# Optimization experiments

Hardware: AMD Instinct MI355X
Metric: run time of the kernel (lower is better)

## Reference

```python
import jax, jax.numpy as jnp
import numpy as np

B, C, H, W = 8, 256, 128, 128


def _conv1x1(x, w, b):
    # x: [B,C,H,W], w: [Cout,Cin], b: [Cout]
    return jnp.einsum('oc,bchw->bohw', w, x) + b[None, :, None, None]


def setup_inputs() -> dict:
    key = jax.random.key(0)
    ks = jax.random.split(key, 12)
    s = 1.0 / np.sqrt(C)
    d = {
        'x0': jax.random.normal(ks[0], (B, C, H, W), jnp.float32),
        'x1': jax.random.normal(ks[1], (B, C, H, W), jnp.float32),
        'g_w': jax.random.uniform(ks[2], (C, C), jnp.float32, -s, s),
        'g_b': jax.random.uniform(ks[3], (C,), jnp.float32, -s, s),
        'theta_w': jax.random.uniform(ks[4], (C, C), jnp.float32, -s, s),
        'theta_b': jax.random.uniform(ks[5], (C,), jnp.float32, -s, s),
        'phi_w': jax.random.uniform(ks[6], (C, C), jnp.float32, -s, s),
        'phi_b': jax.random.uniform(ks[7], (C,), jnp.float32, -s, s),
        # Original inits W to zero; use small random weights so output/grads are nontrivial.
        'W_w': jax.random.uniform(ks[8], (C, C), jnp.float32, -s, s) * 0.1,
        'W_b': jax.random.uniform(ks[9], (C,), jnp.float32, -s, s) * 0.1,
    }
    return d


def reference(x0, x1, g_w, g_b, theta_w, theta_b, phi_w, phi_b, W_w, W_b):
    b, c, h, w = x0.shape
    n = h * w
    g_x = _conv1x1(x0, g_w, g_b).reshape(b, c, n)        # [B,C,N]
    theta_x = _conv1x1(x1, theta_w, theta_b).reshape(b, c, n)  # [B,C,N]
    phi_x = _conv1x1(x0, phi_w, phi_b).reshape(b, c, n)   # [B,C,N]
    # f = theta_x @ phi_x^T : [B,C,C]; NO scaling, softmax over dim=1 (columns-normalized)
    f = jnp.einsum('bcn,bdn->bcd', theta_x, phi_x)
    f_div_C = jax.nn.softmax(f, axis=1)
    y = jnp.einsum('bcd,bdn->bcn', f_div_C, g_x)          # [B,C,N]
    # Faithful to torch: permute to [B,N,C] contiguous, then view as [B,C,H,W]
    y = jnp.transpose(y, (0, 2, 1)).reshape(b, c, h, w)
    return _conv1x1(y, W_w, W_b)
```

## Files before the change

### kernel.cpp

```cpp
#include <hip/hip_runtime.h>
#include <hip/hip_bf16.h>
#include <stdint.h>


typedef __attribute__((ext_vector_type(4))) float f32x4;
typedef __attribute__((ext_vector_type(8))) short s16x8;

#define MFMA16(A,B,C) __builtin_amdgcn_mfma_f32_16x16x32_bf16((A),(B),(C),0,0,0)

__device__ __forceinline__ short f2bf(float f) {
    union { float f; uint32_t u; } v; v.f = f;
    uint32_t r = v.u + 0x7fffu + ((v.u >> 16) & 1u);
    return (short)(r >> 16);
}
__device__ __forceinline__ float bf2f(short h) {
    union { uint32_t u; float f; } v; v.u = ((uint32_t)(uint16_t)h) << 16;
    return v.f;
}
__device__ __forceinline__ s16x8 pack2(f32x4 a, f32x4 b) {
    s16x8 r;
    r[0]=f2bf(a.x); r[1]=f2bf(a.y); r[2]=f2bf(a.z); r[3]=f2bf(a.w);
    r[4]=f2bf(b.x); r[5]=f2bf(b.y); r[6]=f2bf(b.z); r[7]=f2bf(b.w);
    return r;
}
__device__ __forceinline__ void pack2_hl(f32x4 a, f32x4 b, s16x8& hi, s16x8& lo) {
    float v[8] = {a.x,a.y,a.z,a.w,b.x,b.y,b.z,b.w};
#pragma unroll
    for (int i=0;i<8;++i) {
        short h = f2bf(v[i]);
        hi[i] = h;
        lo[i] = f2bf(v[i] - bf2f(h));
    }
}
__device__ __forceinline__ float hsum4(f32x4 v){ return (v.x+v.y)+(v.z+v.w); }

__global__ __launch_bounds__(256) void k0_prep(
    const float* __restrict__ g_w, const float* __restrict__ W_w,
    short* __restrict__ gwT, short* __restrict__ Wwb,
    float* __restrict__ s0, float* __restrict__ s1)
{
    int gid = blockIdx.x * 256 + threadIdx.x;
    int d = gid >> 8, e = gid & 255;
    gwT[e*256 + d] = f2bf(g_w[gid]);
    Wwb[gid] = f2bf(W_w[gid]);
    if (gid < 2048) { s0[gid] = 0.f; s1[gid] = 0.f; }
}

__global__ __launch_bounds__(256) void k1_gram(
    const float* __restrict__ x0, const float* __restrict__ x1,
    float* __restrict__ partial, float* __restrict__ s0, float* __restrict__ s1)
{
    __shared__ short Ah[128*40], Al[128*40], Bh[128*40], Bl[128*40];
    int bid = blockIdx.x;
    int ij = bid & 3, ch = (bid >> 2) & 15, b = bid >> 6;
    int i0 = (ij >> 1) * 128, j0 = (ij & 1) * 128, k0 = ch * 1024;
    int tid = threadIdx.x;
    int w = tid >> 6, lane = tid & 63;
    int wr = (w >> 1) * 64, wc = (w & 1) * 64;
    int quad = lane >> 4, l16 = lane & 15;
    int srow = tid >> 1, skk = (tid & 1) * 16;

    const float* pa = x1 + (size_t)(b*256 + i0 + srow)*16384 + k0 + skk;
    const float* pb = x0 + (size_t)(b*256 + j0 + srow)*16384 + k0 + skk;

    f32x4 acc[4][4];
#pragma unroll
    for (int i=0;i<4;i++)
#pragma unroll
    for (int j=0;j<4;j++) acc[i][j] = f32x4{0.f,0.f,0.f,0.f};

    float sumA = 0.f, sumB = 0.f;

    for (int s = 0; s < 32; ++s) {
        f32x4 av[4], bv[4];
#pragma unroll
        for (int q=0;q<4;++q) { av[q] = *(const f32x4*)(pa + q*4); bv[q] = *(const f32x4*)(pb + q*4); }
        pa += 32; pb += 32;
#pragma unroll
        for (int q=0;q<4;++q) { sumA += hsum4(av[q]); sumB += hsum4(bv[q]); }
        __syncthreads();
        s16x8 h, l;
        pack2_hl(av[0], av[1], h, l);
        ((s16x8*)(Ah + srow*40 + skk))[0] = h; ((s16x8*)(Al + srow*40 + skk))[0] = l;
        pack2_hl(av[2], av[3], h, l);
        ((s16x8*)(Ah + srow*40 + skk))[1] = h; ((s16x8*)(Al + srow*40 + skk))[1] = l;
        pack2_hl(bv[0], bv[1], h, l);
        ((s16x8*)(Bh + srow*40 + skk))[0] = h; ((s16x8*)(Bl + srow*40 + skk))[0] = l;
        pack2_hl(bv[2], bv[3], h, l);
        ((s16x8*)(Bh + srow*40 + skk))[1] = h; ((s16x8*)(Bl + srow*40 + skk))[1] = l;
        __syncthreads();
        s16x8 ah[4], al[4], bh[4], bl[4];
#pragma unroll
        for (int mt=0; mt<4; ++mt) {
            ah[mt] = *(const s16x8*)(Ah + (wr + mt*16 + l16)*40 + quad*8);
            al[mt] = *(const s16x8*)(Al + (wr + mt*16 + l16)*40 + quad*8);
        }
#pragma unroll
        for (int nt=0; nt<4; ++nt) {
            bh[nt] = *(const s16x8*)(Bh + (wc + nt*16 + l16)*40 + quad*8);
            bl[nt] = *(const s16x8*)(Bl + (wc + nt*16 + l16)*40 + quad*8);
        }
#pragma unroll
        for (int mt=0; mt<4; ++mt)
#pragma unroll
        for (int nt=0; nt<4; ++nt) {
            acc[mt][nt] = MFMA16(ah[mt], bh[nt], acc[mt][nt]);
            acc[mt][nt] = MFMA16(ah[mt], bl[nt], acc[mt][nt]);
            acc[mt][nt] = MFMA16(al[mt], bh[nt], acc[mt][nt]);
        }
    }
    float oA = sumA + __shfl_down(sumA, 1);
    float oB = sumB + __shfl_down(sumB, 1);
    if ((tid & 1) == 0) {
        if (j0 == 0) atomicAdd(&s1[b*256 + i0 + srow], oA);
        if (i0 == 0) atomicAdd(&s0[b*256 + j0 + srow], oB);
    }
    float* outp = partial + (size_t)bid * 16384;
#pragma unroll
    for (int mt=0; mt<4; ++mt)
#pragma unroll
    for (int nt=0; nt<4; ++nt)
#pragma unroll
    for (int r=0; r<4; ++r) {
        int row = wr + mt*16 + quad*4 + r;
        int col = wc + nt*16 + l16;
        outp[row*128 + col] = acc[mt][nt][r];
    }
}

__global__ __launch_bounds__(256) void k1_reduce(
    const float* __restrict__ partial, float* __restrict__ M)
{
    int gid = blockIdx.x*256 + threadIdx.x;
    int b = gid >> 16;
    int rem = gid & 65535;
    int i = rem >> 8, j = rem & 255;
    int ij = ((i>>7)<<1) | (j>>7);
    int idx = (i&127)*128 + (j&127);
    float s = 0.f;
#pragma unroll
    for (int ch = 0; ch < 16; ++ch)
        s += partial[(size_t)((b*16 + ch)*4 + ij)*16384 + idx];
    M[gid] = s;
}

__global__ __launch_bounds__(256) void k2m(
    const float* __restrict__ Tw, const float* __restrict__ Pw,
    const float* __restrict__ pb, const float* __restrict__ s0,
    const float* __restrict__ s1, float* __restrict__ SA, float* __restrict__ SP)
{
    __shared__ float sv[256];
    int b = blockIdx.x >> 1, which = blockIdx.x & 1;
    int t = threadIdx.x;
    sv[t] = which ? s0[b*256 + t] : s1[b*256 + t];
    __syncthreads();
    const float* W = which ? Pw : Tw;
    const float* row = W + t*256;
    float acc = 0.f;
    for (int i = 0; i < 256; ++i) acc += row[i] * sv[i];
    if (which) SP[b*256 + t] = acc + 16384.f * pb[t];
    else       SA[b*256 + t] = acc;
}

__global__ __launch_bounds__(256) void k2a(
    const float* __restrict__ Pw, const float* __restrict__ M, float* __restrict__ P1T)
{
    __shared__ short Ah[128*40], Al[128*40], Bh[128*40], Bl[128*40];
    int bid = blockIdx.x;
    int b = bid >> 2, d0 = ((bid>>1)&1)*128, i0 = (bid&1)*128;
    int tid = threadIdx.x;
    int w = tid >> 6, lane = tid & 63;
    int wr = (w >> 1) * 64, wc = (w & 1) * 64;
    int quad = lane >> 4, l16 = lane & 15;
    int srow = tid >> 1, skk = (tid & 1) * 16;

    f32x4 acc[4][4];
#pragma unroll
    for (int i=0;i<4;i++)
#pragma unroll
    for (int j=0;j<4;j++) acc[i][j] = f32x4{0.f,0.f,0.f,0.f};

    for (int s = 0; s < 8; ++s) {
        const float* pa = Pw + (d0 + srow)*256 + s*32 + skk;
        const float* pm = M + (size_t)b*65536 + (i0 + srow)*256 + s*32 + skk;
        f32x4 av[4], bv[4];
#pragma unroll
        for (int q=0;q<4;++q) { av[q] = *(const f32x4*)(pa + q*4); bv[q] = *(const f32x4*)(pm + q*4); }
        __syncthreads();
        s16x8 h, l;
        pack2_hl(av[0], av[1], h, l);
        ((s16x8*)(Ah + srow*40 + skk))[0] = h; ((s16x8*)(Al + srow*40 + skk))[0] = l;
        pack2_hl(av[2], av[3], h, l);
        ((s16x8*)(Ah + srow*40 + skk))[1] = h; ((s16x8*)(Al + srow*40 + skk))[1] = l;
        pack2_hl(bv[0], bv[1], h, l);
        ((s16x8*)(Bh + srow*40 + skk))[0] = h; ((s16x8*)(Bl + srow*40 + skk))[0] = l;
        pack2_hl(bv[2], bv[3], h, l);
        ((s16x8*)(Bh + srow*40 + skk))[1] = h; ((s16x8*)(Bl + srow*40 + skk))[1] = l;
        __syncthreads();
        s16x8 ah[4], al[4], bh[4], bl[4];
#pragma unroll
        for (int mt=0; mt<4; ++mt) {
            ah[mt] = *(const s16x8*)(Ah + (wr + mt*16 + l16)*40 + quad*8);
            al[mt] = *(const s16x8*)(Al + (wr + mt*16 + l16)*40 + quad*8);
        }
#pragma unroll
        for (int nt=0; nt<4; ++nt) {
            bh[nt] = *(const s16x8*)(Bh + (wc + nt*16 + l16)*40 + quad*8);
            bl[nt] = *(const s16x8*)(Bl + (wc + nt*16 + l16)*40 + quad*8);
        }
#pragma unroll
        for (int mt=0; mt<4; ++mt)
#pragma unroll
        for (int nt=0; nt<4; ++nt) {
            acc[mt][nt] = MFMA16(ah[mt], bh[nt], acc[mt][nt]);
            acc[mt][nt] = MFMA16(ah[mt], bl[nt], acc[mt][nt]);
            acc[mt][nt] = MFMA16(al[mt], bh[nt], acc[mt][nt]);
        }
    }
#pragma unroll
    for (int mt=0; mt<4; ++mt)
#pragma unroll
    for (int nt=0; nt<4; ++nt)
#pragma unroll
    for (int r=0; r<4; ++r) {
        int row = wr + mt*16 + quad*4 + r;
        int col = wc + nt*16 + l16;
        P1T[(size_t)b*65536 + (d0+row)*256 + i0 + col] = acc[mt][nt][r];
    }
}

__global__ __launch_bounds__(256) void k2b1(
    const float* __restrict__ Tw, const float* __restrict__ P1T,
    const float* __restrict__ tb, const float* __restrict__ pb,
    const float* __restrict__ SA, const float* __restrict__ SP,
    float* __restrict__ fws)
{
    __shared__ short Ah[256*40], Al[256*40], Bh[64*40], Bl[64*40];
    int bid = blockIdx.x;
    int b = bid >> 2, d0 = (bid & 3)*64;
    int tid = threadIdx.x;
    int w = tid >> 6, lane = tid & 63;
    int quad = lane >> 4, l16 = lane & 15;

    f32x4 acc[4][4];
#pragma unroll
    for (int i=0;i<4;i++)
#pragma unroll
    for (int j=0;j<4;j++) acc[i][j] = f32x4{0.f,0.f,0.f,0.f};

    for (int s = 0; s < 8; ++s) {
        const float* pa = Tw + tid*256 + s*32;
        f32x4 av[8];
#pragma unroll
        for (int q=0;q<8;++q) av[q] = *(const f32x4*)(pa + q*4);
        const float* pbp = P1T + (size_t)b*65536 + (d0 + (tid>>2))*256 + s*32 + (tid&3)*8;
        f32x4 bv0 = *(const f32x4*)(pbp), bv1 = *(const f32x4*)(pbp + 4);
        __syncthreads();
        s16x8 h, l;
#pragma unroll
        for (int q=0;q<4;++q) {
            pack2_hl(av[2*q], av[2*q+1], h, l);
            ((s16x8*)(Ah + tid*40))[q] = h;
            ((s16x8*)(Al + tid*40))[q] = l;
        }
        pack2_hl(bv0, bv1, h, l);
        *(s16x8*)(Bh + (tid>>2)*40 + (tid&3)*8) = h;
        *(s16x8*)(Bl + (tid>>2)*40 + (tid&3)*8) = l;
        __syncthreads();
        s16x8 ah[4], al[4], bh[4], bl[4];
#pragma unroll
        for (int mt=0; mt<4; ++mt) {
            ah[mt] = *(const s16x8*)(Ah + (w*64 + mt*16 + l16)*40 + quad*8);
            al[mt] = *(const s16x8*)(Al + (w*64 + mt*16 + l16)*40 + quad*8);
        }
#pragma unroll
        for (int nt=0; nt<4; ++nt) {
            bh[nt] = *(const s16x8*)(Bh + (nt*16 + l16)*40 + quad*8);
            bl[nt] = *(const s16x8*)(Bl + (nt*16 + l16)*40 + quad*8);
        }
#pragma unroll
        for (int mt=0; mt<4; ++mt)
#pragma unroll
        for (int nt=0; nt<4; ++nt) {
            acc[mt][nt] = MFMA16(ah[mt], bh[nt], acc[mt][nt]);
            acc[mt][nt] = MFMA16(ah[mt], bl[nt], acc[mt][nt]);
            acc[mt][nt] = MFMA16(al[mt], bh[nt], acc[mt][nt]);
        }
    }
#pragma unroll
    for (int mt=0; mt<4; ++mt)
#pragma unroll
    for (int nt=0; nt<4; ++nt)
#pragma unroll
    for (int r=0; r<4; ++r) {
        int c = w*64 + mt*16 + quad*4 + r;
        int d = d0 + nt*16 + l16;
        float fv = acc[mt][nt][r] + tb[c]*SP[b*256 + d] + SA[b*256 + c]*pb[d];
        fws[(size_t)b*65536 + d*256 + c] = fv;
    }
}

__global__ __launch_bounds__(256) void k2b2(
    const float* __restrict__ fws, short* __restrict__ F)
{
    int b = blockIdx.x, d = threadIdx.x;
    const float* fr = fws + (size_t)b*65536 + d*256;
    float mx = -1e30f;
    for (int c=0;c<256;++c) mx = fmaxf(mx, fr[c]);
    float sum = 0.f;
    for (int c=0;c<256;++c) sum += __expf(fr[c] - mx);
    float inv = 1.f / sum;
    for (int c=0;c<256;++c)
        F[(size_t)b*65536 + c*256 + d] = f2bf(__expf(fr[c] - mx) * inv);
}

__global__ __launch_bounds__(256) void k2c(
    const short* __restrict__ F, const short* __restrict__ gwT,
    const float* __restrict__ g_b, short* __restrict__ G, float* __restrict__ yb)
{
    int bid = blockIdx.x;
    int b = bid >> 2, c0 = ((bid>>1)&1)*128, e0 = (bid&1)*128;
    int tid = threadIdx.x;
    int w = tid >> 6, lane = tid & 63;
    int wr = (w >> 1) * 64, wc = (w & 1) * 64;
    int quad = lane >> 4, l16 = lane & 15;

    f32x4 acc[4][4];
#pragma unroll
    for (int i=0;i<4;i++)
#pragma unroll
    for (int j=0;j<4;j++) acc[i][j] = f32x4{0.f,0.f,0.f,0.f};

    for (int s = 0; s < 8; ++s) {
        int k0 = s*32;
        s16x8 af[4], bfr[4];
#pragma unroll
        for (int mt=0; mt<4; ++mt)
            af[mt] = *(const s16x8*)(F + (size_t)b*65536 + (c0 + wr + mt*16 + l16)*256 + k0 + quad*8);
#pragma unroll
        for (int nt=0; nt<4; ++nt)
            bfr[nt] = *(const s16x8*)(gwT + (e0 + wc + nt*16 + l16)*256 + k0 + quad*8);
#pragma unroll
        for (int mt=0; mt<4; ++mt)
#pragma unroll
        for (int nt=0; nt<4; ++nt)
            acc[mt][nt] = MFMA16(af[mt], bfr[nt], acc[mt][nt]);
    }
#pragma unroll
    for (int mt=0; mt<4; ++mt)
#pragma unroll
    for (int nt=0; nt<4; ++nt)
#pragma unroll
    for (int r=0; r<4; ++r) {
        int c = c0 + wr + mt*16 + quad*4 + r;
        int e = e0 + wc + nt*16 + l16;
        G[(size_t)b*65536 + c*256 + e] = f2bf(acc[mt][nt][r]);
    }
    if (e0 == 0 && tid < 128) {
        int c = c0 + tid;
        float a = 0.f;
        const short* fr = F + (size_t)b*65536 + c*256;
        for (int d=0; d<256; ++d) a += bf2f(fr[d]) * g_b[d];
        yb[b*256 + c] = a;
    }
}

__global__ __launch_bounds__(256) void k3a(
    const float* __restrict__ x0, const short* __restrict__ G,
    const float* __restrict__ yb, short* __restrict__ yv)
{
    __shared__ short smX[64*40];
    int bid = blockIdx.x;
    int b = bid >> 8, m0 = (bid & 255) * 64;
    int tid = threadIdx.x;
    int w = tid >> 6, lane = tid & 63;
    int quad = lane >> 4, l16 = lane & 15;
    int rc = w * 64;
    int se = tid >> 3, sm = (tid & 7) * 8;

    const float* px = x0 + (size_t)(b*256 + se)*16384 + m0 + sm;

    f32x4 acc[4][4];
#pragma unroll
    for (int i=0;i<4;i++)
#pragma unroll
    for (int j=0;j<4;j++) acc[i][j] = f32x4{0.f,0.f,0.f,0.f};

    for (int s = 0; s < 8; ++s) {
        int e0 = s*32;
        f32x4 v0 = *(const f32x4*)(px);
        f32x4 v1 = *(const f32x4*)(px + 4);
        px += (size_t)32*16384;
        __syncthreads();
        short hv[8] = {f2bf(v0.x),f2bf(v0.y),f2bf(v0.z),f2bf(v0.w),
                       f2bf(v1.x),f2bf(v1.y),f2bf(v1.z),f2bf(v1.w)};
#pragma unroll
        for (int i=0;i<8;++i) smX[(sm + i)*40 + se] = hv[i];
        __syncthreads();
        s16x8 af[4], bfr[4];
#pragma unroll
        for (int mt=0; mt<4; ++mt)
            af[mt] = *(const s16x8*)(smX + (mt*16 + l16)*40 + quad*8);
#pragma unroll
        for (int nt=0; nt<4; ++nt)
            bfr[nt] = *(const s16x8*)(G + (size_t)b*65536 + (rc + nt*16 + l16)*256 + e0 + quad*8);
#pragma unroll
        for (int mt=0; mt<4; ++mt)
#pragma unroll
        for (int nt=0; nt<4; ++nt)
            acc[mt][nt] = MFMA16(af[mt], bfr[nt], acc[mt][nt]);
    }
    float ybv[4];
#pragma unroll
    for (int nt=0; nt<4; ++nt) ybv[nt] = yb[b*256 + rc + nt*16 + l16];
    short* base = yv + (size_t)b*4194304 + (size_t)m0*256;
#pragma unroll
    for (int mt=0; mt<4; ++mt)
#pragma unroll
    for (int nt=0; nt<4; ++nt)
#pragma unroll
    for (int r=0; r<4; ++r) {
        int m  = mt*16 + quad*4 + r;
        int rr = rc + nt*16 + l16;
        base[m*256 + rr] = f2bf(acc[mt][nt][r] + ybv[nt]);
    }
}

__global__ __launch_bounds__(256) void k3b(
    const short* __restrict__ yv, const short* __restrict__ Wwb,
    const float* __restrict__ W_b, float* __restrict__ out)
{
    __shared__ short smY[128*40];
    int bid = blockIdx.x;
    int b = bid >> 8, rem = bid & 255;
    int o0 = (rem >> 7) * 128, n0 = (rem & 127) * 128;
    int tid = threadIdx.x;
    int w = tid >> 6, lane = tid & 63;
    int wr = (w >> 1) * 64, wc = (w & 1) * 64;
    int quad = lane >> 4, l16 = lane & 15;
    int sc = tid >> 3, sn = (tid & 7) * 16;

    const short* py = yv + (size_t)b*4194304 + (size_t)sc*16384 + n0 + sn;

    f32x4 acc[4][4];
#pragma unroll
    for (int i=0;i<4;i++)
#pragma unroll
    for (int j=0;j<4;j++) acc[i][j] = f32x4{0.f,0.f,0.f,0.f};

    for (int s = 0; s < 8; ++s) {
        int c0 = s*32;
        s16x8 y0 = *(const s16x8*)(py);
        s16x8 y1 = *(const s16x8*)(py + 8);
        py += (size_t)32*16384;
        __syncthreads();
#pragma unroll
        for (int i=0;i<8;++i) { smY[(sn + i)*40 + sc] = y0[i]; smY[(sn + 8 + i)*40 + sc] = y1[i]; }
        __syncthreads();
        s16x8 af[4], bfr[4];
#pragma unroll
        for (int mt=0; mt<4; ++mt)
            af[mt] = *(const s16x8*)(Wwb + (o0 + wr + mt*16 + l16)*256 + c0 + quad*8);
#pragma unroll
        for (int nt=0; nt<4; ++nt)
            bfr[nt] = *(const s16x8*)(smY + (wc + nt*16 + l16)*40 + quad*8);
#pragma unroll
        for (int mt=0; mt<4; ++mt)
#pragma unroll
        for (int nt=0; nt<4; ++nt)
            acc[mt][nt] = MFMA16(af[mt], bfr[nt], acc[mt][nt]);
    }
#pragma unroll
    for (int mt=0; mt<4; ++mt)
#pragma unroll
    for (int nt=0; nt<4; ++nt)
#pragma unroll
    for (int r=0; r<4; ++r) {
        int o  = o0 + wr + mt*16 + quad*4 + r;
        int nn = n0 + wc + nt*16 + l16;
        out[(size_t)(b*256 + o)*16384 + nn] = acc[mt][nt][r] + W_b[o];
    }
}

extern "C" void kernel_launch(void* const* d_in, const int* in_sizes, int n_in,
                              void* d_out, int out_size, void* d_ws, size_t ws_size,
                              hipStream_t stream)
{
    (void)in_sizes; (void)n_in; (void)out_size; (void)ws_size;
    const float* x0   = (const float*)d_in[0];
    const float* x1   = (const float*)d_in[1];
    const float* g_w  = (const float*)d_in[2];
    const float* g_b  = (const float*)d_in[3];
    const float* th_w = (const float*)d_in[4];
    const float* th_b = (const float*)d_in[5];
    const float* ph_w = (const float*)d_in[6];
    const float* ph_b = (const float*)d_in[7];
    const float* W_w  = (const float*)d_in[8];
    const float* W_b  = (const float*)d_in[9];
    float* out = (float*)d_out;

    char* ws = (char*)d_ws;
    short* yv      = (short*)(ws + 0);
    float* partial = (float*)(ws + 0);
    float* M       = (float*)(ws + 67108864);
    float* P1T     = (float*)(ws + 69206016);
    float* fws     = (float*)(ws + 71303168);
    short* F       = (short*)(ws + 73400320);
    short* G       = (short*)(ws + 74448896);
    short* gwT     = (short*)(ws + 75497472);
    short* Wwb     = (short*)(ws + 75628544);
    float* s0      = (float*)(ws + 75759616);
    float* s1      = (float*)(ws + 75767808);
    float* SA      = (float*)(ws + 75776000);
    float* SP      = (float*)(ws + 75784192);
    float* yb      = (float*)(ws + 75792384);

    k0_prep  <<<dim3(256),  dim3(256), 0, stream>>>(g_w, W_w, gwT, Wwb, s0, s1);
    k1_gram  <<<dim3(512),  dim3(256), 0, stream>>>(x0, x1, partial, s0, s1);
    k1_reduce<<<dim3(2048), dim3(256), 0, stream>>>(partial, M);
    k2m      <<<dim3(16),   dim3(256), 0, stream>>>(th_w, ph_w, ph_b, s0, s1, SA, SP);
    k2a      <<<dim3(32),   dim3(256), 0, stream>>>(ph_w, M, P1T);
    k2b1     <<<dim3(32),   dim3(256), 0, stream>>>(th_w, P1T, th_b, ph_b, SA, SP, fws);
    k2b2     <<<dim3(8),    dim3(256), 0, stream>>>(fws, F);
    k2c      <<<dim3(32),   dim3(256), 0, stream>>>(F, gwT, g_b, G, yb);
    k3a      <<<dim3(2048), dim3(256), 0, stream>>>(x0, G, yb, yv);
    k3b      <<<dim3(2048), dim3(256), 0, stream>>>(yv, Wwb, W_b, out);
}
```

Before: 596.5 us.

## Transpose x0 to bf16, add direct-load GEMMs, parallelize softmax, split gram finer

```diff
diff --git a/kernel.cpp b/kernel.cpp
--- a/kernel.cpp
+++ b/kernel.cpp
@@ -17,20 +17,26 @@
     union { uint32_t u; float f; } v; v.u = ((uint32_t)(uint16_t)h) << 16;
     return v.f;
 }
-__device__ __forceinline__ s16x8 pack2(f32x4 a, f32x4 b) {
-    s16x8 r;
-    r[0]=f2bf(a.x); r[1]=f2bf(a.y); r[2]=f2bf(a.z); r[3]=f2bf(a.w);
-    r[4]=f2bf(b.x); r[5]=f2bf(b.y); r[6]=f2bf(b.z); r[7]=f2bf(b.w);
+__device__ __forceinline__ uint32_t cvtpk(float a, float b) {
+    uint32_t r;
+    asm("v_cvt_pk_bf16_f32 %0, %1, %2" : "=v"(r) : "v"(a), "v"(b));
     return r;
 }
 __device__ __forceinline__ void pack2_hl(f32x4 a, f32x4 b, s16x8& hi, s16x8& lo) {
     float v[8] = {a.x,a.y,a.z,a.w,b.x,b.y,b.z,b.w};
-#pragma unroll
-    for (int i=0;i<8;++i) {
-        short h = f2bf(v[i]);
-        hi[i] = h;
-        lo[i] = f2bf(v[i] - bf2f(h));
-    }
+    uint32_t h[4]; float r[8];
+#pragma unroll
+    for (int i=0;i<4;++i) {
+        h[i] = cvtpk(v[2*i], v[2*i+1]);
+        float f0 = __uint_as_float(h[i] << 16);
+        float f1 = __uint_as_float(h[i] & 0xffff0000u);
+        r[2*i]   = v[2*i]   - f0;
+        r[2*i+1] = v[2*i+1] - f1;
+    }
+    union { uint32_t u[4]; s16x8 s; } H, L;
+#pragma unroll
+    for (int i=0;i<4;++i) { H.u[i] = h[i]; L.u[i] = cvtpk(r[2*i], r[2*i+1]); }
+    hi = H.s; lo = L.s;
 }
 __device__ __forceinline__ float hsum4(f32x4 v){ return (v.x+v.y)+(v.z+v.w); }
 
@@ -52,8 +58,8 @@
 {
     __shared__ short Ah[128*40], Al[128*40], Bh[128*40], Bl[128*40];
     int bid = blockIdx.x;
-    int ij = bid & 3, ch = (bid >> 2) & 15, b = bid >> 6;
-    int i0 = (ij >> 1) * 128, j0 = (ij & 1) * 128, k0 = ch * 1024;
+    int ij = bid & 3, ch = (bid >> 2) & 31, b = bid >> 7;
+    int i0 = (ij >> 1) * 128, j0 = (ij & 1) * 128, k0 = ch * 512;
     int tid = threadIdx.x;
     int w = tid >> 6, lane = tid & 63;
     int wr = (w >> 1) * 64, wc = (w & 1) * 64;
@@ -71,7 +77,7 @@
 
     float sumA = 0.f, sumB = 0.f;
 
-    for (int s = 0; s < 32; ++s) {
+    for (int s = 0; s < 16; ++s) {
         f32x4 av[4], bv[4];
 #pragma unroll
         for (int q=0;q<4;++q) { av[q] = *(const f32x4*)(pa + q*4); bv[q] = *(const f32x4*)(pb + q*4); }
@@ -139,9 +145,43 @@
     int idx = (i&127)*128 + (j&127);
     float s = 0.f;
 #pragma unroll
-    for (int ch = 0; ch < 16; ++ch)
-        s += partial[(size_t)((b*16 + ch)*4 + ij)*16384 + idx];
+    for (int ch = 0; ch < 32; ++ch)
+        s += partial[(size_t)((b*32 + ch)*4 + ij)*16384 + idx];
     M[gid] = s;
+}
+
+__global__ __launch_bounds__(256) void kT(
+    const float* __restrict__ x0, short* __restrict__ x0T)
+{
+    __shared__ short sm[64*72];
+    int bid = blockIdx.x;
+    int b = bid >> 10, eb = (bid >> 8) & 3, nb = bid & 255;
+    int e0 = eb*64, n0 = nb*64;
+    int t = threadIdx.x;
+    int eg = t >> 4, np = (t & 15)*4;
+    const float* p0 = x0 + (size_t)(b*256 + e0 + eg*4)*16384 + n0 + np;
+    f32x4 r0 = *(const f32x4*)(p0);
+    f32x4 r1 = *(const f32x4*)(p0 + 16384);
+    f32x4 r2 = *(const f32x4*)(p0 + 32768);
+    f32x4 r3 = *(const f32x4*)(p0 + 49152);
+    float a0[4] = {r0.x,r0.y,r0.z,r0.w};
+    float a1[4] = {r1.x,r1.y,r1.z,r1.w};
+    float a2[4] = {r2.x,r2.y,r2.z,r2.w};
+    float a3[4] = {r3.x,r3.y,r3.z,r3.w};
+#pragma unroll
+    for (int j=0;j<4;++j) {
+        uint32_t u0 = cvtpk(a0[j], a1[j]);
+        uint32_t u1 = cvtpk(a2[j], a3[j]);
+        uint32_t* d = (uint32_t*)(sm + (np+j)*72 + eg*4);
+        d[0] = u0; d[1] = u1;
+    }
+    __syncthreads();
+    int nl = t >> 2, ec = (t & 3)*16;
+    s16x8 w0 = *(const s16x8*)(sm + nl*72 + ec);
+    s16x8 w1 = *(const s16x8*)(sm + nl*72 + ec + 8);
+    short* dst = x0T + (size_t)b*4194304 + (size_t)(nl*256 + nb)*256 + e0 + ec;
+    ((s16x8*)dst)[0] = w0;
+    ((s16x8*)dst)[1] = w1;
 }
 
 __global__ __launch_bounds__(256) void k2m(
@@ -303,15 +343,25 @@
 __global__ __launch_bounds__(256) void k2b2(
     const float* __restrict__ fws, short* __restrict__ F)
 {
-    int b = blockIdx.x, d = threadIdx.x;
+    int b = blockIdx.x >> 6;
+    int d = (blockIdx.x & 63)*4 + (threadIdx.x >> 6);
+    int lane = threadIdx.x & 63;
     const float* fr = fws + (size_t)b*65536 + d*256;
-    float mx = -1e30f;
-    for (int c=0;c<256;++c) mx = fmaxf(mx, fr[c]);
-    float sum = 0.f;
-    for (int c=0;c<256;++c) sum += __expf(fr[c] - mx);
-    float inv = 1.f / sum;
-    for (int c=0;c<256;++c)
-        F[(size_t)b*65536 + c*256 + d] = f2bf(__expf(fr[c] - mx) * inv);
+    float v[4];
+#pragma unroll
+    for (int i=0;i<4;++i) v[i] = fr[lane + i*64];
+    float mx = fmaxf(fmaxf(v[0],v[1]), fmaxf(v[2],v[3]));
+#pragma unroll
+    for (int off=32; off>0; off>>=1) mx = fmaxf(mx, __shfl_xor(mx, off));
+    float s = 0.f;
+#pragma unroll
+    for (int i=0;i<4;++i) { v[i] = __expf(v[i] - mx); s += v[i]; }
+#pragma unroll
+    for (int off=32; off>0; off>>=1) s += __shfl_xor(s, off);
+    float inv = 1.f / s;
+#pragma unroll
+    for (int i=0;i<4;++i)
+        F[(size_t)b*65536 + (size_t)(lane + i*64)*256 + d] = f2bf(v[i] * inv);
 }
 
 __global__ __launch_bounds__(256) void k2c(
@@ -365,6 +415,101 @@
     }
 }
 
+__global__ __launch_bounds__(256) void k3a_f(
+    const short* __restrict__ x0T, const short* __restrict__ G,
+    const float* __restrict__ yb, short* __restrict__ yvT)
+{
+    int bid = blockIdx.x;
+    int b = bid >> 8, r = (bid >> 2) & 63, c0 = ((bid>>1)&1)*128, q0 = (bid&1)*128;
+    int tid = threadIdx.x;
+    int w = tid >> 6, lane = tid & 63;
+    int wr = (w >> 1) * 64, wc = (w & 1) * 64;
+    int quad = lane >> 4, l16 = lane & 15;
+
+    const short* Gb = G + (size_t)b*65536;
+    const short* Xb = x0T + (size_t)b*4194304 + (size_t)r*65536;
+
+    f32x4 acc[4][4];
+#pragma unroll
+    for (int i=0;i<4;i++)
+#pragma unroll
+    for (int j=0;j<4;j++) acc[i][j] = f32x4{0.f,0.f,0.f,0.f};
+
+    for (int s = 0; s < 8; ++s) {
+        int k0 = s*32;
+        s16x8 af[4], bfr[4];
+#pragma unroll
+        for (int mt=0; mt<4; ++mt)
+            af[mt] = *(const s16x8*)(Gb + (c0 + wr + mt*16 + l16)*256 + k0 + quad*8);
+#pragma unroll
+        for (int nt=0; nt<4; ++nt)
+            bfr[nt] = *(const s16x8*)(Xb + (q0 + wc + nt*16 + l16)*256 + k0 + quad*8);
+#pragma unroll
+        for (int mt=0; mt<4; ++mt)
+#pragma unroll
+        for (int nt=0; nt<4; ++nt)
+            acc[mt][nt] = MFMA16(af[mt], bfr[nt], acc[mt][nt]);
+    }
+    short* dst = yvT + (size_t)b*4194304 + (size_t)r*65536;
+#pragma unroll
+    for (int mt=0; mt<4; ++mt)
+#pragma unroll
+    for (int nt=0; nt<4; ++nt)
+#pragma unroll
+    for (int rr=0; rr<4; ++rr) {
+        int c = c0 + wr + mt*16 + quad*4 + rr;
+        int q = q0 + wc + nt*16 + l16;
+        dst[(size_t)c*256 + q] = f2bf(acc[mt][nt][rr] + yb[b*256 + c]);
+    }
+}
+
+__global__ __launch_bounds__(256) void k3b_f(
+    const short* __restrict__ yvT, const short* __restrict__ Wwb,
+    const float* __restrict__ W_b, float* __restrict__ out)
+{
+    int bid = blockIdx.x;
+    int b = bid >> 8, rem = bid & 255;
+    int o0 = (rem >> 7) * 128, n0 = (rem & 127) * 128;
+    int tid = threadIdx.x;
+    int w = tid >> 6, lane = tid & 63;
+    int wr = (w >> 1) * 64, wc = (w & 1) * 64;
+    int quad = lane >> 4, l16 = lane & 15;
+
+    const short* Yb = yvT + (size_t)b*4194304;
+
+    f32x4 acc[4][4];
+#pragma unroll
+    for (int i=0;i<4;i++)
+#pragma unroll
+    for (int j=0;j<4;j++) acc[i][j] = f32x4{0.f,0.f,0.f,0.f};
+
+    for (int s = 0; s < 8; ++s) {
+        int k0 = s*32;
+        s16x8 af[4], bfr[4];
+#pragma unroll
+        for (int mt=0; mt<4; ++mt)
+            af[mt] = *(const s16x8*)(Wwb + (o0 + wr + mt*16 + l16)*256 + k0 + quad*8);
+#pragma unroll
+        for (int nt=0; nt<4; ++nt)
+            bfr[nt] = *(const s16x8*)(Yb + (size_t)(n0 + wc + nt*16 + l16)*256 + k0 + quad*8);
+#pragma unroll
+        for (int mt=0; mt<4; ++mt)
+#pragma unroll
+        for (int nt=0; nt<4; ++nt)
+            acc[mt][nt] = MFMA16(af[mt], bfr[nt], acc[mt][nt]);
+    }
+#pragma unroll
+    for (int mt=0; mt<4; ++mt)
+#pragma unroll
+    for (int nt=0; nt<4; ++nt)
+#pragma unroll
+    for (int r=0; r<4; ++r) {
+        int o  = o0 + wr + mt*16 + quad*4 + r;
+        int nn = n0 + wc + nt*16 + l16;
+        out[(size_t)(b*256 + o)*16384 + nn] = acc[mt][nt][r] + W_b[o];
+    }
+}
+
 __global__ __launch_bounds__(256) void k3a(
     const float* __restrict__ x0, const short* __restrict__ G,
     const float* __restrict__ yb, short* __restrict__ yv)
@@ -486,7 +631,7 @@
                               void* d_out, int out_size, void* d_ws, size_t ws_size,
                               hipStream_t stream)
 {
-    (void)in_sizes; (void)n_in; (void)out_size; (void)ws_size;
+    (void)in_sizes; (void)n_in; (void)out_size;
     const float* x0   = (const float*)d_in[0];
     const float* x1   = (const float*)d_in[1];
     const float* g_w  = (const float*)d_in[2];
@@ -514,15 +659,26 @@
     float* SA      = (float*)(ws + 75776000);
     float* SP      = (float*)(ws + 75784192);
     float* yb      = (float*)(ws + 75792384);
+    short* x0T     = (short*)(ws + 75800576);
+    const size_t WS_NEED_FAST = 75800576u + 67108864u;
+
+    bool fast = (ws_size >= WS_NEED_FAST);
 
     k0_prep  <<<dim3(256),  dim3(256), 0, stream>>>(g_w, W_w, gwT, Wwb, s0, s1);
-    k1_gram  <<<dim3(512),  dim3(256), 0, stream>>>(x0, x1, partial, s0, s1);
+    k1_gram  <<<dim3(1024), dim3(256), 0, stream>>>(x0, x1, partial, s0, s1);
     k1_reduce<<<dim3(2048), dim3(256), 0, stream>>>(partial, M);
+    if (fast)
+        kT   <<<dim3(8192), dim3(256), 0, stream>>>(x0, x0T);
     k2m      <<<dim3(16),   dim3(256), 0, stream>>>(th_w, ph_w, ph_b, s0, s1, SA, SP);
     k2a      <<<dim3(32),   dim3(256), 0, stream>>>(ph_w, M, P1T);
     k2b1     <<<dim3(32),   dim3(256), 0, stream>>>(th_w, P1T, th_b, ph_b, SA, SP, fws);
-    k2b2     <<<dim3(8),    dim3(256), 0, stream>>>(fws, F);
+    k2b2     <<<dim3(512),  dim3(256), 0, stream>>>(fws, F);
     k2c      <<<dim3(32),   dim3(256), 0, stream>>>(F, gwT, g_b, G, yb);
-    k3a      <<<dim3(2048), dim3(256), 0, stream>>>(x0, G, yb, yv);
-    k3b      <<<dim3(2048), dim3(256), 0, stream>>>(yv, Wwb, W_b, out);
-}
+    if (fast) {
+        k3a_f<<<dim3(2048), dim3(256), 0, stream>>>(x0T, G, yb, yv);
+        k3b_f<<<dim3(2048), dim3(256), 0, stream>>>(yv, Wwb, W_b, out);
+    } else {
+        k3a  <<<dim3(2048), dim3(256), 0, stream>>>(x0, G, yb, yv);
+        k3b  <<<dim3(2048), dim3(256), 0, stream>>>(yv, Wwb, W_b, out);
+    }
+}
```

Result: faster. 583.2 us (-2.2%).

## Prefetch global tiles, parallelize softmax, split gram K finer, use hardware bf16 pack

Applied to the files above, without the earlier changes.

```diff
diff --git a/kernel.cpp b/kernel.cpp
--- a/kernel.cpp
+++ b/kernel.cpp
@@ -17,20 +17,26 @@
     union { uint32_t u; float f; } v; v.u = ((uint32_t)(uint16_t)h) << 16;
     return v.f;
 }
-__device__ __forceinline__ s16x8 pack2(f32x4 a, f32x4 b) {
-    s16x8 r;
-    r[0]=f2bf(a.x); r[1]=f2bf(a.y); r[2]=f2bf(a.z); r[3]=f2bf(a.w);
-    r[4]=f2bf(b.x); r[5]=f2bf(b.y); r[6]=f2bf(b.z); r[7]=f2bf(b.w);
+__device__ __forceinline__ uint32_t cvtpk(float a, float b) {
+    uint32_t r;
+    asm("v_cvt_pk_bf16_f32 %0, %1, %2" : "=v"(r) : "v"(a), "v"(b));
     return r;
 }
 __device__ __forceinline__ void pack2_hl(f32x4 a, f32x4 b, s16x8& hi, s16x8& lo) {
     float v[8] = {a.x,a.y,a.z,a.w,b.x,b.y,b.z,b.w};
-#pragma unroll
-    for (int i=0;i<8;++i) {
-        short h = f2bf(v[i]);
-        hi[i] = h;
-        lo[i] = f2bf(v[i] - bf2f(h));
-    }
+    uint32_t h[4]; float r[8];
+#pragma unroll
+    for (int i=0;i<4;++i) {
+        h[i] = cvtpk(v[2*i], v[2*i+1]);
+        float f0 = __uint_as_float(h[i] << 16);
+        float f1 = __uint_as_float(h[i] & 0xffff0000u);
+        r[2*i]   = v[2*i]   - f0;
+        r[2*i+1] = v[2*i+1] - f1;
+    }
+    union { uint32_t u[4]; s16x8 s; } H, L;
+#pragma unroll
+    for (int i=0;i<4;++i) { H.u[i] = h[i]; L.u[i] = cvtpk(r[2*i], r[2*i+1]); }
+    hi = H.s; lo = L.s;
 }
 __device__ __forceinline__ float hsum4(f32x4 v){ return (v.x+v.y)+(v.z+v.w); }
 
@@ -52,8 +58,8 @@
 {
     __shared__ short Ah[128*40], Al[128*40], Bh[128*40], Bl[128*40];
     int bid = blockIdx.x;
-    int ij = bid & 3, ch = (bid >> 2) & 15, b = bid >> 6;
-    int i0 = (ij >> 1) * 128, j0 = (ij & 1) * 128, k0 = ch * 1024;
+    int ij = bid & 3, ch = (bid >> 2) & 31, b = bid >> 7;
+    int i0 = (ij >> 1) * 128, j0 = (ij & 1) * 128, k0 = ch * 512;
     int tid = threadIdx.x;
     int w = tid >> 6, lane = tid & 63;
     int wr = (w >> 1) * 64, wc = (w & 1) * 64;
@@ -71,14 +77,15 @@
 
     float sumA = 0.f, sumB = 0.f;
 
-    for (int s = 0; s < 32; ++s) {
-        f32x4 av[4], bv[4];
-#pragma unroll
-        for (int q=0;q<4;++q) { av[q] = *(const f32x4*)(pa + q*4); bv[q] = *(const f32x4*)(pb + q*4); }
-        pa += 32; pb += 32;
+    f32x4 av[4], bv[4];
+#pragma unroll
+    for (int q=0;q<4;++q) { av[q] = *(const f32x4*)(pa + q*4); bv[q] = *(const f32x4*)(pb + q*4); }
+    pa += 32; pb += 32;
+
+    for (int s = 0; s < 16; ++s) {
+        __syncthreads();
 #pragma unroll
         for (int q=0;q<4;++q) { sumA += hsum4(av[q]); sumB += hsum4(bv[q]); }
-        __syncthreads();
         s16x8 h, l;
         pack2_hl(av[0], av[1], h, l);
         ((s16x8*)(Ah + srow*40 + skk))[0] = h; ((s16x8*)(Al + srow*40 + skk))[0] = l;
@@ -89,6 +96,12 @@
         pack2_hl(bv[2], bv[3], h, l);
         ((s16x8*)(Bh + srow*40 + skk))[1] = h; ((s16x8*)(Bl + srow*40 + skk))[1] = l;
         __syncthreads();
+        f32x4 nav[4], nbv[4];
+        if (s < 15) {
+#pragma unroll
+            for (int q=0;q<4;++q) { nav[q] = *(const f32x4*)(pa + q*4); nbv[q] = *(const f32x4*)(pb + q*4); }
+            pa += 32; pb += 32;
+        }
         s16x8 ah[4], al[4], bh[4], bl[4];
 #pragma unroll
         for (int mt=0; mt<4; ++mt) {
@@ -107,6 +120,10 @@
             acc[mt][nt] = MFMA16(ah[mt], bh[nt], acc[mt][nt]);
             acc[mt][nt] = MFMA16(ah[mt], bl[nt], acc[mt][nt]);
             acc[mt][nt] = MFMA16(al[mt], bh[nt], acc[mt][nt]);
+        }
+        if (s < 15) {
+#pragma unroll
+            for (int q=0;q<4;++q) { av[q] = nav[q]; bv[q] = nbv[q]; }
         }
     }
     float oA = sumA + __shfl_down(sumA, 1);
@@ -139,8 +156,8 @@
     int idx = (i&127)*128 + (j&127);
     float s = 0.f;
 #pragma unroll
-    for (int ch = 0; ch < 16; ++ch)
-        s += partial[(size_t)((b*16 + ch)*4 + ij)*16384 + idx];
+    for (int ch = 0; ch < 32; ++ch)
+        s += partial[(size_t)((b*32 + ch)*4 + ij)*16384 + idx];
     M[gid] = s;
 }
 
@@ -180,12 +197,14 @@
 #pragma unroll
     for (int j=0;j<4;j++) acc[i][j] = f32x4{0.f,0.f,0.f,0.f};
 
+    const float* pa0 = Pw + (d0 + srow)*256 + skk;
+    const float* pm0 = M + (size_t)b*65536 + (i0 + srow)*256 + skk;
+
+    f32x4 av[4], bv[4];
+#pragma unroll
+    for (int q=0;q<4;++q) { av[q] = *(const f32x4*)(pa0 + q*4); bv[q] = *(const f32x4*)(pm0 + q*4); }
+
     for (int s = 0; s < 8; ++s) {
-        const float* pa = Pw + (d0 + srow)*256 + s*32 + skk;
-        const float* pm = M + (size_t)b*65536 + (i0 + srow)*256 + s*32 + skk;
-        f32x4 av[4], bv[4];
-#pragma unroll
-        for (int q=0;q<4;++q) { av[q] = *(const f32x4*)(pa + q*4); bv[q] = *(const f32x4*)(pm + q*4); }
         __syncthreads();
         s16x8 h, l;
         pack2_hl(av[0], av[1], h, l);
@@ -197,6 +216,13 @@
         pack2_hl(bv[2], bv[3], h, l);
         ((s16x8*)(Bh + srow*40 + skk))[1] = h; ((s16x8*)(Bl + srow*40 + skk))[1] = l;
         __syncthreads();
+        f32x4 nav[4], nbv[4];
+        if (s < 7) {
+            const float* pa = pa0 + (s+1)*32;
+            const float* pm = pm0 + (s+1)*32;
+#pragma unroll
+            for (int q=0;q<4;++q) { nav[q] = *(const f32x4*)(pa + q*4); nbv[q] = *(const f32x4*)(pm + q*4); }
+        }
         s16x8 ah[4], al[4], bh[4], bl[4];
 #pragma unroll
         for (int mt=0; mt<4; ++mt) {
@@ -215,6 +241,10 @@
             acc[mt][nt] = MFMA16(ah[mt], bh[nt], acc[mt][nt]);
             acc[mt][nt] = MFMA16(ah[mt], bl[nt], acc[mt][nt]);
             acc[mt][nt] = MFMA16(al[mt], bh[nt], acc[mt][nt]);
+        }
+        if (s < 7) {
+#pragma unroll
+            for (int q=0;q<4;++q) { av[q] = nav[q]; bv[q] = nbv[q]; }
         }
     }
 #pragma unroll
@@ -248,13 +278,15 @@
 #pragma unroll
     for (int j=0;j<4;j++) acc[i][j] = f32x4{0.f,0.f,0.f,0.f};
 
+    const float* pa0 = Tw + tid*256;
+    const float* pb0 = P1T + (size_t)b*65536 + (d0 + (tid>>2))*256 + (tid&3)*8;
+
+    f32x4 av[8]; f32x4 bv0, bv1;
+#pragma unroll
+    for (int q=0;q<8;++q) av[q] = *(const f32x4*)(pa0 + q*4);
+    bv0 = *(const f32x4*)(pb0); bv1 = *(const f32x4*)(pb0 + 4);
+
     for (int s = 0; s < 8; ++s) {
-        const float* pa = Tw + tid*256 + s*32;
-        f32x4 av[8];
-#pragma unroll
-        for (int q=0;q<8;++q) av[q] = *(const f32x4*)(pa + q*4);
-        const float* pbp = P1T + (size_t)b*65536 + (d0 + (tid>>2))*256 + s*32 + (tid&3)*8;
-        f32x4 bv0 = *(const f32x4*)(pbp), bv1 = *(const f32x4*)(pbp + 4);
         __syncthreads();
         s16x8 h, l;
 #pragma unroll
@@ -267,6 +299,14 @@
         *(s16x8*)(Bh + (tid>>2)*40 + (tid&3)*8) = h;
         *(s16x8*)(Bl + (tid>>2)*40 + (tid&3)*8) = l;
         __syncthreads();
+        f32x4 nav[8], nbv0, nbv1;
+        if (s < 7) {
+            const float* pa = pa0 + (s+1)*32;
+            const float* pbp = pb0 + (s+1)*32;
+#pragma unroll
+            for (int q=0;q<8;++q) nav[q] = *(const f32x4*)(pa + q*4);
+            nbv0 = *(const f32x4*)(pbp); nbv1 = *(const f32x4*)(pbp + 4);
+        }
         s16x8 ah[4], al[4], bh[4], bl[4];
 #pragma unroll
         for (int mt=0; mt<4; ++mt) {
@@ -285,6 +325,11 @@
             acc[mt][nt] = MFMA16(ah[mt], bh[nt], acc[mt][nt]);
             acc[mt][nt] = MFMA16(ah[mt], bl[nt], acc[mt][nt]);
             acc[mt][nt] = MFMA16(al[mt], bh[nt], acc[mt][nt]);
+        }
+        if (s < 7) {
+#pragma unroll
+            for (int q=0;q<8;++q) av[q] = nav[q];
+            bv0 = nbv0; bv1 = nbv1;
         }
     }
 #pragma unroll
@@ -303,15 +348,25 @@
 __global__ __launch_bounds__(256) void k2b2(
     const float* __restrict__ fws, short* __restrict__ F)
 {
-    int b = blockIdx.x, d = threadIdx.x;
+    int b = blockIdx.x >> 6;
+    int d = (blockIdx.x & 63)*4 + (threadIdx.x >> 6);
+    int lane = threadIdx.x & 63;
     const float* fr = fws + (size_t)b*65536 + d*256;
-    float mx = -1e30f;
-    for (int c=0;c<256;++c) mx = fmaxf(mx, fr[c]);
-    float sum = 0.f;
-    for (int c=0;c<256;++c) sum += __expf(fr[c] - mx);
-    float inv = 1.f / sum;
-    for (int c=0;c<256;++c)
-        F[(size_t)b*65536 + c*256 + d] = f2bf(__expf(fr[c] - mx) * inv);
+    float v[4];
+#pragma unroll
+    for (int i=0;i<4;++i) v[i] = fr[lane + i*64];
+    float mx = fmaxf(fmaxf(v[0],v[1]), fmaxf(v[2],v[3]));
+#pragma unroll
+    for (int off=32; off>0; off>>=1) mx = fmaxf(mx, __shfl_xor(mx, off));
+    float s = 0.f;
+#pragma unroll
+    for (int i=0;i<4;++i) { v[i] = __expf(v[i] - mx); s += v[i]; }
+#pragma unroll
+    for (int off=32; off>0; off>>=1) s += __shfl_xor(s, off);
+    float inv = 1.f / s;
+#pragma unroll
+    for (int i=0;i<4;++i)
+        F[(size_t)b*65536 + (size_t)(lane + i*64)*256 + d] = f2bf(v[i] * inv);
 }
 
 __global__ __launch_bounds__(256) void k2c(
@@ -376,9 +431,13 @@
     int w = tid >> 6, lane = tid & 63;
     int quad = lane >> 4, l16 = lane & 15;
     int rc = w * 64;
-    int se = tid >> 3, sm = (tid & 7) * 8;
-
-    const float* px = x0 + (size_t)(b*256 + se)*16384 + m0 + sm;
+    int se2 = tid >> 4;
+    int g   = tid & 15;
+    int keyw = (g >> 1) & 3;
+
+    const float* px = x0 + (size_t)(b*256 + 2*se2)*16384 + m0 + 4*g;
+    const short* Gb = G + (size_t)b*65536;
+    uint32_t* smDW = (uint32_t*)smX;
 
     f32x4 acc[4][4];
 #pragma unroll
@@ -386,29 +445,51 @@
 #pragma unroll
     for (int j=0;j<4;j++) acc[i][j] = f32x4{0.f,0.f,0.f,0.f};
 
+    f32x4 xr0 = *(const f32x4*)(px);
+    f32x4 xr1 = *(const f32x4*)(px + 16384);
+    px += (size_t)32*16384;
+    s16x8 bfr[4];
+#pragma unroll
+    for (int nt=0; nt<4; ++nt)
+        bfr[nt] = *(const s16x8*)(Gb + (rc + nt*16 + l16)*256 + quad*8);
+
     for (int s = 0; s < 8; ++s) {
-        int e0 = s*32;
-        f32x4 v0 = *(const f32x4*)(px);
-        f32x4 v1 = *(const f32x4*)(px + 4);
-        px += (size_t)32*16384;
-        __syncthreads();
-        short hv[8] = {f2bf(v0.x),f2bf(v0.y),f2bf(v0.z),f2bf(v0.w),
-                       f2bf(v1.x),f2bf(v1.y),f2bf(v1.z),f2bf(v1.w)};
-#pragma unroll
-        for (int i=0;i<8;++i) smX[(sm + i)*40 + se] = hv[i];
-        __syncthreads();
-        s16x8 af[4], bfr[4];
-#pragma unroll
-        for (int mt=0; mt<4; ++mt)
-            af[mt] = *(const s16x8*)(smX + (mt*16 + l16)*40 + quad*8);
-#pragma unroll
-        for (int nt=0; nt<4; ++nt)
-            bfr[nt] = *(const s16x8*)(G + (size_t)b*65536 + (rc + nt*16 + l16)*256 + e0 + quad*8);
+        __syncthreads();
+        float a0[4] = {xr0.x, xr0.y, xr0.z, xr0.w};
+        float a1[4] = {xr1.x, xr1.y, xr1.z, xr1.w};
+#pragma unroll
+        for (int j=0;j<4;++j) {
+            uint32_t u = cvtpk(a0[j], a1[j]);
+            smDW[(4*g + j)*20 + (se2 ^ (keyw << 2))] = u;
+        }
+        __syncthreads();
+        f32x4 nx0, nx1; s16x8 nbf[4];
+        if (s < 7) {
+            nx0 = *(const f32x4*)(px);
+            nx1 = *(const f32x4*)(px + 16384);
+            px += (size_t)32*16384;
+            int e0 = (s+1)*32;
+#pragma unroll
+            for (int nt=0; nt<4; ++nt)
+                nbf[nt] = *(const s16x8*)(Gb + (rc + nt*16 + l16)*256 + e0 + quad*8);
+        }
+        s16x8 af[4];
+#pragma unroll
+        for (int mt=0; mt<4; ++mt) {
+            int row = mt*16 + l16;
+            int kk  = (row >> 3) & 3;
+            af[mt] = *(const s16x8*)(smX + row*40 + 8*(quad ^ kk));
+        }
 #pragma unroll
         for (int mt=0; mt<4; ++mt)
 #pragma unroll
         for (int nt=0; nt<4; ++nt)
             acc[mt][nt] = MFMA16(af[mt], bfr[nt], acc[mt][nt]);
+        if (s < 7) {
+            xr0 = nx0; xr1 = nx1;
+#pragma unroll
+            for (int nt=0; nt<4; ++nt) bfr[nt] = nbf[nt];
+        }
     }
     float ybv[4];
 #pragma unroll
@@ -438,9 +519,12 @@
     int w = tid >> 6, lane = tid & 63;
     int wr = (w >> 1) * 64, wc = (w & 1) * 64;
     int quad = lane >> 4, l16 = lane & 15;
-    int sc = tid >> 3, sn = (tid & 7) * 16;
-
-    const short* py = yv + (size_t)b*4194304 + (size_t)sc*16384 + n0 + sn;
+    int p   = tid >> 4;
+    int nvg = tid & 15;
+    int keyw = nvg & 3;
+
+    const short* py = yv + (size_t)b*4194304 + (size_t)(2*p)*16384 + n0 + nvg*8;
+    uint32_t* smDW = (uint32_t*)smY;
 
     f32x4 acc[4][4];
 #pragma unroll
@@ -448,27 +532,49 @@
 #pragma unroll
     for (int j=0;j<4;j++) acc[i][j] = f32x4{0.f,0.f,0.f,0.f};
 
+    s16x8 y0 = *(const s16x8*)(py);
+    s16x8 y1 = *(const s16x8*)(py + 16384);
+    py += (size_t)32*16384;
+    s16x8 af[4];
+#pragma unroll
+    for (int mt=0; mt<4; ++mt)
+        af[mt] = *(const s16x8*)(Wwb + (o0 + wr + mt*16 + l16)*256 + quad*8);
+
     for (int s = 0; s < 8; ++s) {
-        int c0 = s*32;
-        s16x8 y0 = *(const s16x8*)(py);
-        s16x8 y1 = *(const s16x8*)(py + 8);
-        py += (size_t)32*16384;
-        __syncthreads();
-#pragma unroll
-        for (int i=0;i<8;++i) { smY[(sn + i)*40 + sc] = y0[i]; smY[(sn + 8 + i)*40 + sc] = y1[i]; }
-        __syncthreads();
-        s16x8 af[4], bfr[4];
-#pragma unroll
-        for (int mt=0; mt<4; ++mt)
-            af[mt] = *(const s16x8*)(Wwb + (o0 + wr + mt*16 + l16)*256 + c0 + quad*8);
-#pragma unroll
-        for (int nt=0; nt<4; ++nt)
-            bfr[nt] = *(const s16x8*)(smY + (wc + nt*16 + l16)*40 + quad*8);
+        __syncthreads();
+#pragma unroll
+        for (int j=0;j<8;++j) {
+            uint32_t u = ((uint32_t)(uint16_t)y0[j]) | ((uint32_t)(uint16_t)y1[j] << 16);
+            smDW[(nvg*8 + j)*20 + (p ^ (keyw << 2))] = u;
+        }
+        __syncthreads();
+        s16x8 ny0, ny1, naf[4];
+        if (s < 7) {
+            ny0 = *(const s16x8*)(py);
+            ny1 = *(const s16x8*)(py + 16384);
+            py += (size_t)32*16384;
+            int c0 = (s+1)*32;
+#pragma unroll
+            for (int mt=0; mt<4; ++mt)
+                naf[mt] = *(const s16x8*)(Wwb + (o0 + wr + mt*16 + l16)*256 + c0 + quad*8);
+        }
+        s16x8 bfr[4];
+#pragma unroll
+        for (int nt=0; nt<4; ++nt) {
+            int nv = wc + nt*16 + l16;
+            int kk = (nv >> 3) & 3;
+            bfr[nt] = *(const s16x8*)(smY + nv*40 + 8*(quad ^ kk));
+        }
 #pragma unroll
         for (int mt=0; mt<4; ++mt)
 #pragma unroll
         for (int nt=0; nt<4; ++nt)
             acc[mt][nt] = MFMA16(af[mt], bfr[nt], acc[mt][nt]);
+        if (s < 7) {
+            y0 = ny0; y1 = ny1;
+#pragma unroll
+            for (int mt=0; mt<4; ++mt) af[mt] = naf[mt];
+        }
     }
 #pragma unroll
     for (int mt=0; mt<4; ++mt)
@@ -516,12 +622,12 @@
     float* yb      = (float*)(ws + 75792384);
 
     k0_prep  <<<dim3(256),  dim3(256), 0, stream>>>(g_w, W_w, gwT, Wwb, s0, s1);
-    k1_gram  <<<dim3(512),  dim3(256), 0, stream>>>(x0, x1, partial, s0, s1);
+    k1_gram  <<<dim3(1024), dim3(256), 0, stream>>>(x0, x1, partial, s0, s1);
     k1_reduce<<<dim3(2048), dim3(256), 0, stream>>>(partial, M);
     k2m      <<<dim3(16),   dim3(256), 0, stream>>>(th_w, ph_w, ph_b, s0, s1, SA, SP);
     k2a      <<<dim3(32),   dim3(256), 0, stream>>>(ph_w, M, P1T);
     k2b1     <<<dim3(32),   dim3(256), 0, stream>>>(th_w, P1T, th_b, ph_b, SA, SP, fws);
-    k2b2     <<<dim3(8),    dim3(256), 0, stream>>>(fws, F);
+    k2b2     <<<dim3(512),  dim3(256), 0, stream>>>(fws, F);
     k2c      <<<dim3(32),   dim3(256), 0, stream>>>(F, gwT, g_b, G, yb);
     k3a      <<<dim3(2048), dim3(256), 0, stream>>>(x0, G, yb, yv);
     k3b      <<<dim3(2048), dim3(256), 0, stream>>>(yv, Wwb, W_b, out);
```

New measurement: 532.8 us. 10.7% less time.
